# Kernel optimization log

Measured on AMD Instinct MI355X. Metric: run time of the kernel, lower is better.

Reference implementation:

```python
import jax, jax.numpy as jnp
import numpy as np

B = 16384; T = 12; MLP = 1024; ZD = 32; H = 128; NSG = 4
N_STATE = 6; NPRED = 2; DT = 0.4 * 4


def _linear_init(k, out_d, in_d):
    s = 1.0 / np.sqrt(in_d)
    kw, kb = jax.random.split(k)
    W = jax.random.uniform(kw, (out_d, in_d), minval=-s, maxval=s, dtype=jnp.float32)
    b = jax.random.uniform(kb, (out_d,), minval=-s, maxval=s, dtype=jnp.float32)
    return W, b


def setup_inputs() -> dict:
    key = jax.random.key(0)
    ks = jax.random.split(key, 16)
    W_dec_hidden, b_dec_hidden = _linear_init(ks[0], H, MLP + ZD)
    W_to_vel, b_to_vel = _linear_init(ks[1], NPRED, N_STATE)
    W_ih, b_ih = _linear_init(ks[2], 3 * H, MLP + ZD + 2 * NPRED)
    W_hh, b_hh = _linear_init(ks[3], 3 * H, H)
    W_mu, b_mu = _linear_init(ks[4], NPRED, H)
    W_std, b_std = _linear_init(ks[5], NPRED, H)
    W_sg, b_sg = _linear_init(ks[6], NPRED, 4)
    return {
        'last_obs_st': jax.random.normal(ks[7], (B, N_STATE), dtype=jnp.float32),
        'last_obs_pos': jax.random.normal(ks[8], (B, 2), dtype=jnp.float32),
        'enc_h_feat': jax.random.normal(ks[9], (B, MLP), dtype=jnp.float32),
        'z': jax.random.normal(ks[10], (B, ZD), dtype=jnp.float32),
        'sg': jax.random.normal(ks[11], (B, NSG, 2), dtype=jnp.float32),
        'fut_traj': jax.random.normal(ks[12], (T, B, N_STATE), dtype=jnp.float32),
        'sg_update_idx': jnp.array([0, 3, 7, 11], dtype=jnp.int32),
        'W_dec_hidden': W_dec_hidden, 'b_dec_hidden': b_dec_hidden,
        'W_to_vel': W_to_vel, 'b_to_vel': b_to_vel,
        'W_ih': W_ih, 'b_ih': b_ih, 'W_hh': W_hh, 'b_hh': b_hh,
        'W_mu': W_mu, 'b_mu': b_mu, 'W_std': W_std, 'b_std': b_std,
        'W_sg': W_sg, 'b_sg': b_sg,
    }


def reference(last_obs_st, last_obs_pos, enc_h_feat, z, sg, fut_traj, sg_update_idx,
              W_dec_hidden, b_dec_hidden, W_to_vel, b_to_vel, W_ih, b_ih,
              W_hh, b_hh, W_mu, b_mu, W_std, b_std, W_sg, b_sg):
    upd = np.asarray(sg_update_idx)  # static control-flow schedule
    zx = jnp.concatenate([enc_h_feat, z], axis=1)              # [B, MLP+ZD]
    h0 = zx @ W_dec_hidden.T + b_dec_hidden                    # [B, H]
    a0 = last_obs_st @ W_to_vel.T + b_to_vel                   # [B, 2]

    pts = jnp.concatenate([last_obs_pos[:, None], sg], axis=1)  # [B, 1+NSG, 2]
    pts = (pts - pts[:, :1]) / 100.0
    v = (pts[:, 1:] - pts[:, :-1]) / DT                         # [B, NSG, 2]
    sg_state = jnp.concatenate([pts[:, 1:], v], axis=-1)        # [B, NSG, 4]
    sg_feat_upd = jnp.einsum('bjf,of->jbo', sg_state, W_sg) + b_sg  # [NSG, B, 2]

    # sg_feat held constant between update steps (matches python-loop gating)
    j_idx = np.clip(np.searchsorted(upd, np.arange(T), side='right') - 1, 0, len(upd) - 1)
    sg_feat_all = sg_feat_upd[j_idx]                            # [T, B, 2]

    # teacher forcing: a for step i>0 is fut_traj[i-1,:,2:4]
    a_seq = jnp.concatenate([a0[None], fut_traj[:-1, :, 2:4]], axis=0)  # [T, B, 2]

    # precompute input-side GRU gate projections (zx part is step-invariant)
    D = zx.shape[1]
    gates_zx = zx @ W_ih[:, :D].T                               # [B, 3H]
    gates_a = jnp.einsum('tbi,gi->tbg', a_seq, W_ih[:, D:D + 2])
    gates_sg = jnp.einsum('tbi,gi->tbg', sg_feat_all, W_ih[:, D + 2:])
    gates_x = gates_zx[None] + gates_a + gates_sg + b_ih        # [T, B, 3H]

    def step(h, gx):
        gh = h @ W_hh.T + b_hh
        r = jax.nn.sigmoid(gx[:, :H] + gh[:, :H])
        zg = jax.nn.sigmoid(gx[:, H:2 * H] + gh[:, H:2 * H])
        n = jnp.tanh(gx[:, 2 * H:] + r * gh[:, 2 * H:])
        h_new = (1.0 - zg) * n + zg * h
        mu = h_new @ W_mu.T + b_mu
        std = jnp.sqrt(jnp.exp(h_new @ W_std.T + b_std))
        return h_new, (mu, std)

    _, (mus, stds) = jax.lax.scan(step, h0, gates_x)
    return mus, stds  # each [T, B, 2] — params of returned Normal
```

## Files before the change

### kernel.cpp

```cpp
#include <hip/hip_runtime.h>
#include <hip/hip_bf16.h>

#define BN 16384
#define TT 12
#define MLP 1024
#define ZD 32
#define HD 128
#define KD 1056
#define GN 384
#define WIH_LD 1060
#define NSG 4
#define DTC 1.6f
#define PLD 512
#define SLD 40
#define GRU_ROWS 16

typedef __attribute__((ext_vector_type(8))) short short8;
typedef __attribute__((ext_vector_type(4))) short short4_t;
typedef __attribute__((ext_vector_type(4))) float floatx4;
typedef __hip_bfloat16 bf16;

__device__ __forceinline__ float bf2f(bf16 v) { return __bfloat162float(v); }
__device__ __forceinline__ bf16 f2bf(float v) { return __float2bfloat16(v); }
__device__ __forceinline__ short bfbits(float x) {
    bf16 t = __float2bfloat16(x);
    return __builtin_bit_cast(short, t);
}
__device__ __forceinline__ float bfraw2f(unsigned short u) {
    return __uint_as_float(((unsigned int)u) << 16);
}
__device__ __forceinline__ float sigm(float x) {
    return __builtin_amdgcn_rcpf(1.0f + __expf(-x));
}
__device__ __forceinline__ float tanh_f(float x) {
    return 1.0f - 2.0f * __builtin_amdgcn_rcpf(1.0f + __expf(2.0f * x));
}
__device__ __forceinline__ short8 pack8(floatx4 a, floatx4 b) {
    short8 v;
    v[0]=bfbits(a[0]); v[1]=bfbits(a[1]); v[2]=bfbits(a[2]); v[3]=bfbits(a[3]);
    v[4]=bfbits(b[0]); v[5]=bfbits(b[1]); v[6]=bfbits(b[2]); v[7]=bfbits(b[3]);
    return v;
}
__device__ __forceinline__ short8 ld8f(const float* q) {
    return pack8(*(const floatx4*)q, *(const floatx4*)(q + 4));
}
__device__ __forceinline__ void barrier_lgkm() {
    asm volatile("s_waitcnt lgkmcnt(0)\n\ts_barrier" ::: "memory");
}

__global__ __launch_bounds__(512, 4) void k_gemm(
    const float* __restrict__ enc, const float* __restrict__ zz,
    const float* __restrict__ Wih, const float* __restrict__ Wdec,
    bf16* __restrict__ P)
{
    __shared__ __align__(16) bf16 sA[2][128 * SLD];
    __shared__ __align__(16) bf16 sB[2][128 * SLD];
    const int tid = threadIdx.x;
    const int lane = tid & 63;
    const int wav = tid >> 6;
    const int wm2 = wav >> 2;
    const int wn2 = wav & 3;
    const int c = lane & 15;
    const int quad = lane >> 4;
    const int m0 = blockIdx.x * 128;
    const int n0 = blockIdx.y * 128;

    const int srow = tid >> 2;
    const int scq = (tid & 3) * 8;
    const int nn = n0 + srow;
    const float* arow = enc + (size_t)(m0 + srow) * MLP + scq;
    const float* zrow = zz + (size_t)(m0 + srow) * ZD + scq;
    const float* brow = (nn < GN) ? Wih + (size_t)nn * WIH_LD + scq
                                  : Wdec + (size_t)(nn - GN) * KD + scq;

    floatx4 pa[2][2], pb[2][2];
#pragma unroll
    for (int s0 = 0; s0 < 2; s0++) {
        const float* qa = arow + s0 * 32;
        const float* qb = brow + s0 * 32;
        pa[s0][0] = *(const floatx4*)qa; pa[s0][1] = *(const floatx4*)(qa + 4);
        pb[s0][0] = *(const floatx4*)qb; pb[s0][1] = *(const floatx4*)(qb + 4);
    }

    floatx4 acc[4][2];
#pragma unroll
    for (int i = 0; i < 4; i++)
#pragma unroll
        for (int j = 0; j < 2; j++) acc[i][j] = floatx4{0.f, 0.f, 0.f, 0.f};

    for (int kc = 0; kc < 33; kc++) {
        const int sl = kc & 1;
        *(short8*)&sA[sl][srow * SLD + scq] = pack8(pa[sl][0], pa[sl][1]);
        *(short8*)&sB[sl][srow * SLD + scq] = pack8(pb[sl][0], pb[sl][1]);
        if (kc + 2 < 33) {
            const int k2 = (kc + 2) * 32;
            const float* qa = (kc + 2 < 32) ? arow + k2 : zrow;
            const float* qb = brow + k2;
            pa[sl][0] = *(const floatx4*)qa; pa[sl][1] = *(const floatx4*)(qa + 4);
            pb[sl][0] = *(const floatx4*)qb; pb[sl][1] = *(const floatx4*)(qb + 4);
        }
        barrier_lgkm();
        short8 a[4], b[2];
#pragma unroll
        for (int i = 0; i < 4; i++)
            a[i] = *(const short8*)&sA[sl][(wm2 * 64 + i * 16 + c) * SLD + quad * 8];
#pragma unroll
        for (int j = 0; j < 2; j++)
            b[j] = *(const short8*)&sB[sl][(wn2 * 32 + j * 16 + c) * SLD + quad * 8];
#pragma unroll
        for (int i = 0; i < 4; i++)
#pragma unroll
            for (int j = 0; j < 2; j++)
                acc[i][j] = __builtin_amdgcn_mfma_f32_16x16x32_bf16(
                    a[i], b[j], acc[i][j], 0, 0, 0);
    }
#pragma unroll
    for (int i = 0; i < 4; i++)
#pragma unroll
        for (int j = 0; j < 2; j++)
#pragma unroll
            for (int r = 0; r < 4; r++)
                P[(size_t)(m0 + wm2 * 64 + i * 16 + quad * 4 + r) * PLD
                  + n0 + wn2 * 32 + j * 16 + c] = f2bf(acc[i][j][r]);
}

struct SMem {
    bf16 h[2][GRU_ROWS][136];
    bf16 ext[TT][GRU_ROWS][4];
    float sgf[NSG][GRU_ROWS][2];
    float a0[GRU_ROWS][2];
    float muw[4][132];
    float b4[4];
};

__device__ __forceinline__ void heads_out(const SMem& s, float* __restrict__ out,
                                          int rows0, int t, int buf, int tid) {
    const int row = tid >> 2;
    const int sel = tid & 3;
    float sum = 0.0f;
#pragma unroll
    for (int k8 = 0; k8 < 16; k8++) {
        short8 hv = *(const short8*)(&s.h[buf][row][k8 * 8]);
#pragma unroll
        for (int u = 0; u < 8; u++)
            sum += bfraw2f((unsigned short)hv[u]) * s.muw[sel][k8 * 8 + u];
    }
    sum += s.b4[sel];
    const size_t TB2 = (size_t)TT * BN * 2;
    const size_t grow = (size_t)rows0 + row;
    if (sel < 2) out[((size_t)t * BN + grow) * 2 + sel] = sum;
    else out[TB2 + ((size_t)t * BN + grow) * 2 + (sel - 2)] = __expf(0.5f * sum);
}

__global__ __launch_bounds__(256, 2) void k_gru(
    const float* __restrict__ lst, const float* __restrict__ lpos,
    const float* __restrict__ sg, const float* __restrict__ fut,
    const int* __restrict__ updp,
    const float* __restrict__ bdec,
    const float* __restrict__ Wtv, const float* __restrict__ btv,
    const float* __restrict__ Wih, const float* __restrict__ bih,
    const float* __restrict__ Whh, const float* __restrict__ bhh,
    const float* __restrict__ Wmu, const float* __restrict__ bmu,
    const float* __restrict__ Wstd, const float* __restrict__ bstd,
    const float* __restrict__ Wsg, const float* __restrict__ bsg,
    const bf16* __restrict__ P, float* __restrict__ out)
{
    __shared__ __align__(16) SMem s;
    const int tid = threadIdx.x;
    const int lane = tid & 63;
    const int wav = tid >> 6;
    const int c = lane & 15;
    const int quad = lane >> 4;
    const int rows0 = blockIdx.x * GRU_ROWS;
    const int jb = wav * 32;

#pragma unroll
    for (int u = tid; u < 512; u += 256) {
        int sel = u >> 7, k = u & 127;
        s.muw[sel][k] = (sel < 2) ? Wmu[sel * 128 + k] : Wstd[(sel - 2) * 128 + k];
    }
    if (tid < 4) s.b4[tid] = (tid < 2) ? bmu[tid] : bstd[tid - 2];
    if (tid < GRU_ROWS) {
        const int row = rows0 + tid;
        for (int pp = 0; pp < 2; pp++) {
            float sum = btv[pp];
            for (int f = 0; f < 6; f++)
                sum += lst[(size_t)row * 6 + f] * Wtv[pp * 6 + f];
            s.a0[tid][pp] = sum;
        }
        float px = lpos[(size_t)row * 2];
        float py = lpos[(size_t)row * 2 + 1];
        float prevx = 0.f, prevy = 0.f;
        for (int j = 0; j < NSG; j++) {
            float rx = (sg[((size_t)row * NSG + j) * 2] - px) * 0.01f;
            float ry = (sg[((size_t)row * NSG + j) * 2 + 1] - py) * 0.01f;
            float vx = (rx - prevx) * (1.0f / DTC), vy = (ry - prevy) * (1.0f / DTC);
            prevx = rx; prevy = ry;
            float st4[4] = {rx, ry, vx, vy};
            for (int pp = 0; pp < 2; pp++) {
                float sum = bsg[pp];
                for (int f = 0; f < 4; f++) sum += st4[f] * Wsg[pp * 4 + f];
                s.sgf[j][tid][pp] = sum;
            }
        }
    }
    int upd[4];
#pragma unroll
    for (int i = 0; i < 4; i++) upd[i] = updp[i];

    short8 Wb[2][3][4];
    short8 Wb4[2][2];
    float Wa2[2][2], Ws2[2][2], bhh2[2];
#pragma unroll
    for (int jt2 = 0; jt2 < 2; jt2++) {
#pragma unroll
        for (int g = 0; g < 3; g++) {
            const int n = g * 128 + jb + jt2 * 16 + c;
#pragma unroll
            for (int kc = 0; kc < 4; kc++)
                Wb[jt2][g][kc] = ld8f(Whh + (size_t)n * HD + kc * 32 + quad * 8);
            if (g < 2) {
                short8 v = {0, 0, 0, 0, 0, 0, 0, 0};
                if (quad == 0) {
                    const float* q = Wih + (size_t)n * WIH_LD + KD;
                    v[0] = bfbits(q[0]); v[1] = bfbits(q[1]);
                    v[2] = bfbits(q[2]); v[3] = bfbits(q[3]);
                }
                Wb4[jt2][g] = v;
            }
        }
        const int n2 = 256 + jb + jt2 * 16 + c;
        const float* q2 = Wih + (size_t)n2 * WIH_LD + KD;
        Wa2[jt2][0] = q2[0]; Wa2[jt2][1] = q2[1];
        Ws2[jt2][0] = q2[2]; Ws2[jt2][1] = q2[3];
        bhh2[jt2] = bhh[n2];
    }

    __syncthreads();

    floatx4 gzx[2][3];
#pragma unroll
    for (int jt2 = 0; jt2 < 2; jt2++) {
#pragma unroll
        for (int g = 0; g < 3; g++) {
            const int n = g * 128 + jb + jt2 * 16 + c;
            float bias = bih[n] + ((g < 2) ? bhh[n] : 0.0f);
            floatx4 v;
#pragma unroll
            for (int r = 0; r < 4; r++) {
                const int mrow = quad * 4 + r;
                v[r] = bf2f(P[(size_t)(rows0 + mrow) * PLD + n]) + bias;
            }
            gzx[jt2][g] = v;
        }
    }
    float hreg[2][4];
#pragma unroll
    for (int jt2 = 0; jt2 < 2; jt2++) {
        const int hcol = jb + jt2 * 16 + c;
        float bd = bdec[hcol];
#pragma unroll
        for (int r = 0; r < 4; r++) {
            const int mrow = quad * 4 + r;
            float hv = bf2f(P[(size_t)(rows0 + mrow) * PLD + GN + hcol]) + bd;
            hreg[jt2][r] = hv;
            s.h[1][mrow][hcol] = f2bf(hv);
        }
    }
    if (tid < TT * GRU_ROWS) {
        const int t = tid >> 4, row = tid & (GRU_ROWS - 1);
        float a0v, a1v;
        if (t == 0) { a0v = s.a0[row][0]; a1v = s.a0[row][1]; }
        else {
            const float* fp = fut + ((size_t)(t - 1) * BN + rows0 + row) * 6 + 2;
            a0v = fp[0]; a1v = fp[1];
        }
        int jj = 0;
#pragma unroll
        for (int q = 1; q < NSG; q++) if (upd[q] <= t) jj = q;
        s.ext[t][row][0] = f2bf(a0v);
        s.ext[t][row][1] = f2bf(a1v);
        s.ext[t][row][2] = f2bf(s.sgf[jj][row][0]);
        s.ext[t][row][3] = f2bf(s.sgf[jj][row][1]);
    }
    __syncthreads();

    for (int t = 0; t < TT; t++) {
        const int bi = (t & 1) ^ 1;
        const int bo = t & 1;

        floatx4 acc[2][3];
#pragma unroll
        for (int jt2 = 0; jt2 < 2; jt2++) {
            acc[jt2][0] = gzx[jt2][0];
            acc[jt2][1] = gzx[jt2][1];
            floatx4 bb; bb[0] = bb[1] = bb[2] = bb[3] = bhh2[jt2];
            acc[jt2][2] = bb;
        }
#pragma unroll
        for (int kc = 0; kc < 4; kc++) {
            short8 am = *(const short8*)(&s.h[bi][c][kc * 32 + quad * 8]);
#pragma unroll
            for (int jt2 = 0; jt2 < 2; jt2++)
#pragma unroll
                for (int g = 0; g < 3; g++)
                    acc[jt2][g] = __builtin_amdgcn_mfma_f32_16x16x32_bf16(
                        am, Wb[jt2][g][kc], acc[jt2][g], 0, 0, 0);
        }
        {
            short8 am4 = {0, 0, 0, 0, 0, 0, 0, 0};
            if (quad == 0) {
                short4_t e = *(const short4_t*)(&s.ext[t][c][0]);
                am4[0] = e[0]; am4[1] = e[1]; am4[2] = e[2]; am4[3] = e[3];
            }
#pragma unroll
            for (int jt2 = 0; jt2 < 2; jt2++)
#pragma unroll
                for (int g = 0; g < 2; g++)
                    acc[jt2][g] = __builtin_amdgcn_mfma_f32_16x16x32_bf16(
                        am4, Wb4[jt2][g], acc[jt2][g], 0, 0, 0);
        }

        if (t > 0 && tid < 64) heads_out(s, out, rows0, t - 1, bi, tid);

#pragma unroll
        for (int r = 0; r < 4; r++) {
            const int mrow = quad * 4 + r;
            short4_t e4 = *(const short4_t*)(&s.ext[t][mrow][0]);
            float a0v = bfraw2f((unsigned short)e4[0]);
            float a1v = bfraw2f((unsigned short)e4[1]);
            float s0v = bfraw2f((unsigned short)e4[2]);
            float s1v = bfraw2f((unsigned short)e4[3]);
#pragma unroll
            for (int jt2 = 0; jt2 < 2; jt2++) {
                float rr = sigm(acc[jt2][0][r]);
                float zg = sigm(acc[jt2][1][r]);
                float tn = a0v * Wa2[jt2][0] + a1v * Wa2[jt2][1]
                         + s0v * Ws2[jt2][0] + s1v * Ws2[jt2][1];
                float narg = gzx[jt2][2][r] + tn + rr * acc[jt2][2][r];
                float nn = tanh_f(narg);
                float hv = nn + zg * (hreg[jt2][r] - nn);
                hreg[jt2][r] = hv;
                s.h[bo][mrow][jb + jt2 * 16 + c] = f2bf(hv);
            }
        }
        barrier_lgkm();
    }
    if (tid < 64) heads_out(s, out, rows0, TT - 1, (TT - 1) & 1, tid);
}

extern "C" void kernel_launch(void* const* d_in, const int* in_sizes, int n_in,
                              void* d_out, int out_size, void* d_ws, size_t ws_size,
                              hipStream_t stream) {
    const float* lst  = (const float*)d_in[0];
    const float* lpos = (const float*)d_in[1];
    const float* enc  = (const float*)d_in[2];
    const float* zz   = (const float*)d_in[3];
    const float* sg   = (const float*)d_in[4];
    const float* fut  = (const float*)d_in[5];
    const int*   upd  = (const int*)d_in[6];
    const float* Wdec = (const float*)d_in[7];
    const float* bdec = (const float*)d_in[8];
    const float* Wtv  = (const float*)d_in[9];
    const float* btv  = (const float*)d_in[10];
    const float* Wih  = (const float*)d_in[11];
    const float* bih  = (const float*)d_in[12];
    const float* Whh  = (const float*)d_in[13];
    const float* bhh  = (const float*)d_in[14];
    const float* Wmu  = (const float*)d_in[15];
    const float* bmu  = (const float*)d_in[16];
    const float* Wstd = (const float*)d_in[17];
    const float* bstd = (const float*)d_in[18];
    const float* Wsg  = (const float*)d_in[19];
    const float* bsg  = (const float*)d_in[20];
    float* out = (float*)d_out;

    bf16* P = (bf16*)d_ws;
    k_gemm<<<dim3(128, 4), 512, 0, stream>>>(enc, zz, Wih, Wdec, P);
    k_gru<<<BN / GRU_ROWS, 256, 0, stream>>>(
        lst, lpos, sg, fut, upd, bdec, Wtv, btv, Wih, bih, Whh, bhh,
        Wmu, bmu, Wstd, bstd, Wsg, bsg, P, out);
}
```

Baseline: 268.1 us.

## Fold biases into GEMM epilogue and stage P rows through LDS in GRU

```diff
diff --git a/kernel.cpp b/kernel.cpp
--- a/kernel.cpp
+++ b/kernel.cpp
@@ -51,6 +51,8 @@
 __global__ __launch_bounds__(512, 4) void k_gemm(
     const float* __restrict__ enc, const float* __restrict__ zz,
     const float* __restrict__ Wih, const float* __restrict__ Wdec,
+    const float* __restrict__ bih, const float* __restrict__ bhh,
+    const float* __restrict__ bdec,
     bf16* __restrict__ P)
 {
     __shared__ __align__(16) bf16 sA[2][128 * SLD];
@@ -82,6 +84,13 @@
         pb[s0][0] = *(const floatx4*)qb; pb[s0][1] = *(const floatx4*)(qb + 4);
     }
 
+    float bias[2];
+#pragma unroll
+    for (int j = 0; j < 2; j++) {
+        const int n = n0 + wn2 * 32 + j * 16 + c;
+        bias[j] = (n < GN) ? (bih[n] + (n < 256 ? bhh[n] : 0.0f)) : bdec[n - GN];
+    }
+
     floatx4 acc[4][2];
 #pragma unroll
     for (int i = 0; i < 4; i++)
@@ -121,10 +130,11 @@
 #pragma unroll
             for (int r = 0; r < 4; r++)
                 P[(size_t)(m0 + wm2 * 64 + i * 16 + quad * 4 + r) * PLD
-                  + n0 + wn2 * 32 + j * 16 + c] = f2bf(acc[i][j][r]);
+                  + n0 + wn2 * 32 + j * 16 + c] = f2bf(acc[i][j][r] + bias[j]);
 }
 
 struct SMem {
+    bf16 pst[GRU_ROWS][520];
     bf16 h[2][GRU_ROWS][136];
     bf16 ext[TT][GRU_ROWS][4];
     float sgf[NSG][GRU_ROWS][2];
@@ -156,9 +166,8 @@
     const float* __restrict__ lst, const float* __restrict__ lpos,
     const float* __restrict__ sg, const float* __restrict__ fut,
     const int* __restrict__ updp,
-    const float* __restrict__ bdec,
     const float* __restrict__ Wtv, const float* __restrict__ btv,
-    const float* __restrict__ Wih, const float* __restrict__ bih,
+    const float* __restrict__ Wih,
     const float* __restrict__ Whh, const float* __restrict__ bhh,
     const float* __restrict__ Wmu, const float* __restrict__ bmu,
     const float* __restrict__ Wstd, const float* __restrict__ bstd,
@@ -171,8 +180,19 @@
     const int wav = tid >> 6;
     const int c = lane & 15;
     const int quad = lane >> 4;
-    const int rows0 = blockIdx.x * GRU_ROWS;
+    const int d = blockIdx.x;
+    const int b = 8 * (d & 7) + 64 * (d >> 6) + ((d >> 3) & 7);
+    const int rows0 = b * GRU_ROWS;
     const int jb = wav * 32;
+
+#pragma unroll
+    for (int it = 0; it < 4; it++) {
+        const int idx = it * 256 + tid;
+        const int row = idx >> 6;
+        const int col8 = idx & 63;
+        *(short8*)&s.pst[row][col8 * 8] =
+            *(const short8*)&P[(size_t)(rows0 + row) * PLD + col8 * 8];
+    }
 
 #pragma unroll
     for (int u = tid; u < 512; u += 256) {
@@ -244,12 +264,11 @@
 #pragma unroll
         for (int g = 0; g < 3; g++) {
             const int n = g * 128 + jb + jt2 * 16 + c;
-            float bias = bih[n] + ((g < 2) ? bhh[n] : 0.0f);
             floatx4 v;
 #pragma unroll
             for (int r = 0; r < 4; r++) {
                 const int mrow = quad * 4 + r;
-                v[r] = bf2f(P[(size_t)(rows0 + mrow) * PLD + n]) + bias;
+                v[r] = bf2f(s.pst[mrow][n]);
             }
             gzx[jt2][g] = v;
         }
@@ -258,11 +277,10 @@
 #pragma unroll
     for (int jt2 = 0; jt2 < 2; jt2++) {
         const int hcol = jb + jt2 * 16 + c;
-        float bd = bdec[hcol];
 #pragma unroll
         for (int r = 0; r < 4; r++) {
             const int mrow = quad * 4 + r;
-            float hv = bf2f(P[(size_t)(rows0 + mrow) * PLD + GN + hcol]) + bd;
+            float hv = bf2f(s.pst[mrow][GN + hcol]);
             hreg[jt2][r] = hv;
             s.h[1][mrow][hcol] = f2bf(hv);
         }
@@ -376,8 +394,8 @@
     float* out = (float*)d_out;
 
     bf16* P = (bf16*)d_ws;
-    k_gemm<<<dim3(128, 4), 512, 0, stream>>>(enc, zz, Wih, Wdec, P);
+    k_gemm<<<dim3(128, 4), 512, 0, stream>>>(enc, zz, Wih, Wdec, bih, bhh, bdec, P);
     k_gru<<<BN / GRU_ROWS, 256, 0, stream>>>(
-        lst, lpos, sg, fut, upd, bdec, Wtv, btv, Wih, bih, Whh, bhh,
+        lst, lpos, sg, fut, upd, Wtv, btv, Wih, Whh, bhh,
         Wmu, bmu, Wstd, bstd, Wsg, bsg, P, out);
 }
```

New measurement: 255.1 us. -4.9%, faster.
